# Performance work log

Measured on AMD Instinct MI355X. Metric: run time of the kernel, lower is better.

Reference implementation:

```python
import jax, jax.numpy as jnp
import numpy as np

ALPHA = 0.2  # LeakyReLU negative slope (undefined global `alpha` in source; canonical GAT value)
MASK_VAL = -9e15


def setup_inputs() -> dict:
    key = jax.random.key(0)
    k = jax.random.split(key, 6)
    B, N, D = 8, 2048, 256
    x = jax.random.normal(k[0], (B, N, D), dtype=jnp.float32)
    adj = jax.random.randint(k[1], (B, N, N), 0, 2, dtype=jnp.int32)
    W = jax.random.normal(k[2], (D, D), dtype=jnp.float32) * (1.414 / np.sqrt(D))
    a = jax.random.normal(k[3], (2 * D, 1), dtype=jnp.float32) * 0.1
    han_w = jax.random.normal(k[4], (D, D), dtype=jnp.float32) / np.sqrt(D)
    han_b = jax.random.normal(k[5], (D,), dtype=jnp.float32) * 0.01
    return {"x": x, "adj": adj, "W": W, "a": a, "han_w": han_w, "han_b": han_b}


def reference(x, adj, W, a, han_w, han_b):
    B, N, D = x.shape
    h = jnp.matmul(x, W)                              # [B,N,D]
    a1 = jnp.matmul(x, a[:D])                         # [B,N,1]
    a2 = jnp.matmul(x, a[D:])                         # [B,N,1]
    # e[b,i,j] = leakyrelu(a1[b,i] + a2[b,j])
    e = jax.nn.leaky_relu(a1 + jnp.swapaxes(a2, 1, 2), negative_slope=ALPHA)  # [B,N,N]
    att = jnp.where(adj > 0, e, MASK_VAL)
    # NOTE: source softmaxes over dim=1 (source-node axis), faithfully reproduced
    att = jax.nn.softmax(att, axis=1)
    h_prime = jnp.matmul(att, h)                      # [B,N,D]
    hid = jax.nn.elu(h_prime)                         # concat=True branch
    return jnp.matmul(hid, han_w) + han_b
```

## Files before the change

### kernel.cpp

```cpp
#include <hip/hip_runtime.h>
#include <hip/hip_bf16.h>
#include <stdint.h>

#define B_ 8
#define N_ 2048
#define D_ 256
#define BN (B_*N_)
#define NSEG 64
#define SROWS (N_/NSEG)

typedef __bf16 bf16;
typedef bf16 bf16x8 __attribute__((ext_vector_type(8)));
typedef bf16 bf16x4 __attribute__((ext_vector_type(4)));
typedef float f32x4 __attribute__((ext_vector_type(4)));

__device__ __forceinline__ void gload16(const void* g, void* l) {
  __builtin_amdgcn_global_load_lds(
      (const __attribute__((address_space(1))) unsigned int*)g,
      (__attribute__((address_space(3))) unsigned int*)l,
      16, 0, 0);
}

__global__ __launch_bounds__(256) void k_transpose_w(
    const float* __restrict__ w, const float* __restrict__ hw,
    bf16* __restrict__ wt, bf16* __restrict__ hwt) {
  int t = blockIdx.x * 256 + threadIdx.x;
  int d = t >> 8, k = t & 255;
  wt[t]  = (bf16)w[k * D_ + d];
  hwt[t] = (bf16)hw[k * D_ + d];
}

__global__ __launch_bounds__(256) void k_gemm_h(
    const float* __restrict__ x, const bf16* __restrict__ wt,
    const float* __restrict__ avec, bf16* __restrict__ hT,
    float* __restrict__ a1, float* __restrict__ e1, float* __restrict__ f1,
    float* __restrict__ a2, float* __restrict__ e2, float* __restrict__ f2) {
  int blk = blockIdx.x;
  int b = blk >> 5;
  int j0 = (blk & 31) * 64;
  int w = threadIdx.x >> 6, l = threadIdx.x & 63;
  int jr = j0 + w * 16 + (l & 15);
  const float* xrow = x + ((size_t)(b * N_ + jr)) * D_;
  int koff = 8 * (l >> 4);
  f32x4 acc[16];
  #pragma unroll
  for (int i = 0; i < 16; ++i) acc[i] = f32x4{0.f, 0.f, 0.f, 0.f};
  float s1 = 0.f, s2 = 0.f;
  for (int kb = 0; kb < D_; kb += 32) {
    float4 xa = *(const float4*)(xrow + kb + koff);
    float4 xb = *(const float4*)(xrow + kb + koff + 4);
    float4 ua = *(const float4*)(avec + kb + koff);
    float4 ub = *(const float4*)(avec + kb + koff + 4);
    float4 va = *(const float4*)(avec + D_ + kb + koff);
    float4 vb = *(const float4*)(avec + D_ + kb + koff + 4);
    s1 = fmaf(xa.x, ua.x, fmaf(xa.y, ua.y, fmaf(xa.z, ua.z, fmaf(xa.w, ua.w, s1))));
    s1 = fmaf(xb.x, ub.x, fmaf(xb.y, ub.y, fmaf(xb.z, ub.z, fmaf(xb.w, ub.w, s1))));
    s2 = fmaf(xa.x, va.x, fmaf(xa.y, va.y, fmaf(xa.z, va.z, fmaf(xa.w, va.w, s2))));
    s2 = fmaf(xb.x, vb.x, fmaf(xb.y, vb.y, fmaf(xb.z, vb.z, fmaf(xb.w, vb.w, s2))));
    bf16x8 af = { (bf16)xa.x, (bf16)xa.y, (bf16)xa.z, (bf16)xa.w,
                  (bf16)xb.x, (bf16)xb.y, (bf16)xb.z, (bf16)xb.w };
    #pragma unroll
    for (int dt = 0; dt < 16; ++dt) {
      bf16x8 bfr = *(const bf16x8*)(wt + (dt * 16 + (l & 15)) * D_ + kb + koff);
      acc[dt] = __builtin_amdgcn_mfma_f32_16x16x32_bf16(af, bfr, acc[dt], 0, 0, 0);
    }
  }
  s1 += __shfl_xor(s1, 16); s1 += __shfl_xor(s1, 32);
  s2 += __shfl_xor(s2, 16); s2 += __shfl_xor(s2, 32);
  if (l < 16) {
    int row = b * N_ + j0 + w * 16 + l;
    a1[row] = s1; e1[row] = __expf(s1); f1[row] = __expf(0.2f * s1);
    a2[row] = s2; e2[row] = __expf(s2); f2[row] = __expf(0.2f * s2);
  }
  int jw = j0 + w * 16 + (l >> 4) * 4;
  #pragma unroll
  for (int dt = 0; dt < 16; ++dt) {
    int d = dt * 16 + (l & 15);
    bf16x4 o = { (bf16)acc[dt][0], (bf16)acc[dt][1], (bf16)acc[dt][2], (bf16)acc[dt][3] };
    *(bf16x4*)(hT + ((size_t)(b * D_ + d)) * N_ + jw) = o;
  }
}

__global__ __launch_bounds__(256) void k_colstats(
    const int* __restrict__ adj,
    const float* __restrict__ a1, const float* __restrict__ e1, const float* __restrict__ f1,
    const float* __restrict__ a2,
    float* __restrict__ partA, float* __restrict__ partB,
    unsigned char* __restrict__ maskB) {
  int blk = blockIdx.x;
  int b  = blk >> 6;
  int is = blk & (NSEG - 1);
  int t = threadIdx.x;
  int ibase = is * SROWS;
  __shared__ float a1s[SROWS], e1s[SROWS], f1s[SROWS];
  if (t < SROWS) {
    int gi = b * N_ + ibase + t;
    a1s[t] = a1[gi]; e1s[t] = e1[gi]; f1s[t] = f1[gi];
  }
  __syncthreads();
  int j0 = t * 8;
  float4 a2lo = *(const float4*)(a2 + b * N_ + j0);
  float4 a2hi = *(const float4*)(a2 + b * N_ + j0 + 4);
  float a2v[8] = {a2lo.x, a2lo.y, a2lo.z, a2lo.w, a2hi.x, a2hi.y, a2hi.z, a2hi.w};
  float SA[8], SB[8];
  #pragma unroll
  for (int e = 0; e < 8; ++e) { SA[e] = 0.f; SB[e] = 0.f; }
  const int* arow = adj + ((size_t)(b * N_ + ibase)) * N_ + j0;
  unsigned char* mrow = maskB + (size_t)(b * N_ + ibase) * (N_ / 8) + t;
  #pragma unroll 4
  for (int ii = 0; ii < SROWS; ++ii) {
    int4 v0 = *(const int4*)(arow + (size_t)ii * N_);
    int4 v1 = *(const int4*)(arow + (size_t)ii * N_ + 4);
    float a1i = a1s[ii], e1i = e1s[ii], f1i = f1s[ii];
    int vals[8] = {v0.x, v0.y, v0.z, v0.w, v1.x, v1.y, v1.z, v1.w};
    unsigned int mb = 0;
    #pragma unroll
    for (int e = 0; e < 8; ++e) {
      bool pred = vals[e] != 0;
      mb |= pred ? (1u << e) : 0u;
      float tt = a1i + a2v[e];
      bool gt = tt > 0.f;
      SA[e] += (pred && gt)  ? e1i : 0.f;
      SB[e] += (pred && !gt) ? f1i : 0.f;
    }
    mrow[(size_t)ii * (N_ / 8)] = (unsigned char)mb;
  }
  float* pA = partA + ((size_t)(b * NSEG + is)) * N_ + j0;
  float* pB = partB + ((size_t)(b * NSEG + is)) * N_ + j0;
  *(float4*)(pA)     = float4{SA[0], SA[1], SA[2], SA[3]};
  *(float4*)(pA + 4) = float4{SA[4], SA[5], SA[6], SA[7]};
  *(float4*)(pB)     = float4{SB[0], SB[1], SB[2], SB[3]};
  *(float4*)(pB + 4) = float4{SB[4], SB[5], SB[6], SB[7]};
}

__global__ __launch_bounds__(256) void k_colfin(
    const float* __restrict__ partA, const float* __restrict__ partB,
    const float* __restrict__ e2, const float* __restrict__ f2,
    float* __restrict__ e2rs, float* __restrict__ f2rs) {
  int g = blockIdx.x * 256 + threadIdx.x;
  int b = g >> 11, j = g & (N_ - 1);
  float SA = 0.f, SB = 0.f;
  #pragma unroll 8
  for (int is = 0; is < NSEG; ++is) {
    SA += partA[((size_t)(b * NSEG + is)) * N_ + j];
    SB += partB[((size_t)(b * NSEG + is)) * N_ + j];
  }
  float s = e2[g] * SA + f2[g] * SB;
  float rs = s > 0.f ? 1.f / s : 0.f;
  e2rs[g] = e2[g] * rs;
  f2rs[g] = f2[g] * rs;
}

__global__ __launch_bounds__(512, 2) void k_attmm(
    const bf16* __restrict__ hT, const unsigned char* __restrict__ maskB,
    const float* __restrict__ a1v, const float* __restrict__ e1v, const float* __restrict__ f1v,
    const float* __restrict__ a2v, const float* __restrict__ e2rs, const float* __restrict__ f2rs,
    const bf16* __restrict__ hwt, const float* __restrict__ hb,
    float* __restrict__ out) {
  __shared__ __attribute__((aligned(128))) char smem[120 * 1024];
  char* s_b = smem;
  char* s_a = smem + 65536;
  float* s_src = (float*)(smem + 81920);
  unsigned char* s_mask = (unsigned char*)(smem + 106496);
  char* s_hid = smem;

  int blk = blockIdx.x;
  int b  = blk & 7;
  int i0 = (blk >> 3) * 64;
  int t = threadIdx.x, w = t >> 6, l = t & 63;
  int l15 = l & 15, lg = l >> 4;
  int iw = w & 1, dw = w >> 1;

  #pragma unroll
  for (int s = 0; s < 3; ++s) {
    int idx = t + s * 512;
    int arr = idx >> 9, pos = (idx & 511) * 4;
    const float* src = (arr == 0) ? (a2v + b * N_) : (arr == 1) ? (e2rs + b * N_) : (f2rs + b * N_);
    *(float4*)(s_src + arr * N_ + pos) = *(const float4*)(src + pos);
  }
  {
    int row = t >> 3, seg = t & 7;
    const unsigned long long* g = (const unsigned long long*)
        (maskB + ((size_t)(b * N_ + i0 + row)) * (N_ / 8) + seg * 32);
    int sw = (row & 31) << 3;
    #pragma unroll
    for (int k2 = 0; k2 < 4; ++k2) {
      int cb = seg * 32 + k2 * 8;
      *(unsigned long long*)(s_mask + row * 256 + (cb ^ sw)) = g[k2];
    }
  }

  int ib = t >> 3, jq = t & 7;
  int gi = b * N_ + i0 + ib;
  float a1i = a1v[gi], e1i = e1v[gi], f1i = f1v[gi];
  int mswz = (ib & 31) << 3;
  const unsigned char* mline = s_mask + ib * 256;
  const bf16* hTb = hT + (size_t)b * D_ * N_;

  f32x4 acc[2][4];
  #pragma unroll
  for (int is = 0; is < 2; ++is)
    #pragma unroll
    for (int ds = 0; ds < 4; ++ds) acc[is][ds] = f32x4{0.f, 0.f, 0.f, 0.f};

  __syncthreads();

  #define STAGE_B(KB, NB) do {                                              \
    char* dstb = s_b + (NB) * 32768;                                        \
    _Pragma("unroll")                                                       \
    for (int r = 0; r < 4; ++r) {                                           \
      int c = r * 512 + t;                                                  \
      int dd = c >> 3, sub = c & 7;                                         \
      int ssub = sub ^ (dd & 7);                                            \
      gload16(hTb + (size_t)dd * N_ + (KB) + ssub * 8, dstb + c * 16);      \
    }                                                                       \
  } while (0)

  #define BUILD_A(KB, NB) do {                                              \
    int jb = (KB) + jq * 8;                                                 \
    float4 p0 = *(const float4*)(s_src + jb);                               \
    float4 p1 = *(const float4*)(s_src + jb + 4);                           \
    float4 q0 = *(const float4*)(s_src + N_ + jb);                          \
    float4 q1 = *(const float4*)(s_src + N_ + jb + 4);                      \
    float4 r0 = *(const float4*)(s_src + 2 * N_ + jb);                      \
    float4 r1 = *(const float4*)(s_src + 2 * N_ + jb + 4);                  \
    unsigned int m = mline[((((KB) >> 3) + jq)) ^ mswz];                    \
    float a2x[8] = {p0.x,p0.y,p0.z,p0.w,p1.x,p1.y,p1.z,p1.w};               \
    float evx[8] = {q0.x,q0.y,q0.z,q0.w,q1.x,q1.y,q1.z,q1.w};               \
    float fvx[8] = {r0.x,r0.y,r0.z,r0.w,r1.x,r1.y,r1.z,r1.w};               \
    bf16x8 av;                                                              \
    _Pragma("unroll")                                                       \
    for (int e = 0; e < 8; ++e) {                                           \
      float tt = a1i + a2x[e];                                              \
      bool sel = tt > 0.f;                                                  \
      float vv = (sel ? e1i : f1i) * (sel ? evx[e] : fvx[e]);               \
      vv = ((m >> e) & 1u) ? vv : 0.f;                                      \
      av[e] = (bf16)vv;                                                     \
    }                                                                       \
    *(bf16x8*)(s_a + (NB) * 8192 + ib * 128 + ((jq ^ (ib & 7)) * 16)) = av; \
  } while (0)

  STAGE_B(0, 0);
  BUILD_A(0, 0);
  __syncthreads();

  int cur = 0;
  for (int ks = 0; ks < 32; ++ks) {
    if (ks < 31) {
      int kbn = (ks + 1) * 64;
      STAGE_B(kbn, cur ^ 1);
      BUILD_A(kbn, cur ^ 1);
    }
    const char* sa = s_a + cur * 8192;
    const char* sb = s_b + cur * 32768;
    #pragma unroll
    for (int kh = 0; kh < 2; ++kh) {
      int kq = kh * 4 + lg;
      bf16x8 afr[2], bfr[4];
      #pragma unroll
      for (int is = 0; is < 2; ++is) {
        int ra = iw * 32 + is * 16 + l15;
        afr[is] = *(const bf16x8*)(sa + ra * 128 + ((kq ^ (ra & 7)) * 16));
      }
      #pragma unroll
      for (int ds = 0; ds < 4; ++ds) {
        int rb = dw * 64 + ds * 16 + l15;
        bfr[ds] = *(const bf16x8*)(sb + rb * 128 + ((kq ^ (rb & 7)) * 16));
      }
      #pragma unroll
      for (int is = 0; is < 2; ++is)
        #pragma unroll
        for (int ds = 0; ds < 4; ++ds)
          acc[is][ds] = __builtin_amdgcn_mfma_f32_16x16x32_bf16(
              afr[is], bfr[ds], acc[is][ds], 0, 0, 0);
    }
    __syncthreads();
    cur ^= 1;
  }

  #pragma unroll
  for (int is = 0; is < 2; ++is) {
    #pragma unroll
    for (int ds = 0; ds < 4; ++ds) {
      int d = dw * 64 + ds * 16 + l15;
      int c = d >> 3, dby = (d & 7) * 2;
      #pragma unroll
      for (int r = 0; r < 4; ++r) {
        int il = iw * 32 + is * 16 + lg * 4 + r;
        float vv = acc[is][ds][r];
        float hv = vv > 0.f ? vv : __expf(vv) - 1.f;
        *(bf16*)(s_hid + il * 512 + ((c ^ (il & 31)) * 16) + dby) = (bf16)hv;
      }
    }
  }
  __syncthreads();

  f32x4 acc2[2][4];
  #pragma unroll
  for (int is = 0; is < 2; ++is)
    #pragma unroll
    for (int ds = 0; ds < 4; ++ds) acc2[is][ds] = f32x4{0.f, 0.f, 0.f, 0.f};
  #pragma unroll
  for (int kh = 0; kh < 8; ++kh) {
    int kc = kh * 4 + lg;
    bf16x8 afr2[2];
    #pragma unroll
    for (int is = 0; is < 2; ++is) {
      int ra = iw * 32 + is * 16 + l15;
      afr2[is] = *(const bf16x8*)(s_hid + ra * 512 + ((kc ^ (ra & 31)) * 16));
    }
    #pragma unroll
    for (int ds = 0; ds < 4; ++ds) {
      int d2 = dw * 64 + ds * 16 + l15;
      bf16x8 bfr2 = *(const bf16x8*)(hwt + (size_t)d2 * D_ + kh * 32 + lg * 8);
      #pragma unroll
      for (int is = 0; is < 2; ++is)
        acc2[is][ds] = __builtin_amdgcn_mfma_f32_16x16x32_bf16(
            afr2[is], bfr2, acc2[is][ds], 0, 0, 0);
    }
  }
  #pragma unroll
  for (int is = 0; is < 2; ++is) {
    #pragma unroll
    for (int ds = 0; ds < 4; ++ds) {
      int d = dw * 64 + ds * 16 + l15;
      float bias = hb[d];
      #pragma unroll
      for (int r = 0; r < 4; ++r) {
        int i = i0 + iw * 32 + is * 16 + lg * 4 + r;
        out[((size_t)(b * N_ + i)) * D_ + d] = acc2[is][ds][r] + bias;
      }
    }
  }
}

extern "C" void kernel_launch(void* const* d_in, const int* in_sizes, int n_in,
                              void* d_out, int out_size, void* d_ws, size_t ws_size,
                              hipStream_t stream) {
  (void)in_sizes; (void)n_in; (void)out_size; (void)ws_size;
  const float* x   = (const float*)d_in[0];
  const int*   adj = (const int*)d_in[1];
  const float* W   = (const float*)d_in[2];
  const float* a   = (const float*)d_in[3];
  const float* hw  = (const float*)d_in[4];
  const float* hb  = (const float*)d_in[5];
  float* out = (float*)d_out;

  char* ws = (char*)d_ws;
  size_t off = 0;
  auto alloc = [&](size_t bytes) -> char* {
    char* p = ws + off;
    off += (bytes + 255) & ~(size_t)255;
    return p;
  };
  float* a1   = (float*)alloc(BN * 4);
  float* e1   = (float*)alloc(BN * 4);
  float* f1   = (float*)alloc(BN * 4);
  float* a2   = (float*)alloc(BN * 4);
  float* e2   = (float*)alloc(BN * 4);
  float* f2   = (float*)alloc(BN * 4);
  float* e2rs = (float*)alloc(BN * 4);
  float* f2rs = (float*)alloc(BN * 4);
  float* partA = (float*)alloc((size_t)B_ * NSEG * N_ * 4);
  float* partB = (float*)alloc((size_t)B_ * NSEG * N_ * 4);
  unsigned char* maskB = (unsigned char*)alloc((size_t)BN * (N_ / 8));
  bf16* hT  = (bf16*)alloc((size_t)B_ * D_ * N_ * 2);
  bf16* wt  = (bf16*)alloc((size_t)D_ * D_ * 2);
  bf16* hwt = (bf16*)alloc((size_t)D_ * D_ * 2);

  k_transpose_w<<<256, 256, 0, stream>>>(W, hw, wt, hwt);
  k_gemm_h<<<256, 256, 0, stream>>>(x, wt, a, hT, a1, e1, f1, a2, e2, f2);
  k_colstats<<<B_ * NSEG, 256, 0, stream>>>(adj, a1, e1, f1, a2, partA, partB, maskB);
  k_colfin<<<BN / 256, 256, 0, stream>>>(partA, partB, e2, f2, e2rs, f2rs);
  k_attmm<<<256, 512, 0, stream>>>(hT, maskB, a1, e1, f1, a2, e2rs, f2rs,
                                   hwt, hb, out);
}
```

Before: 111.3 us.

## Split attention matmul K across warp halves with LDS reduction

Changes the warp tiling of the main attention×h MFMA loop. Each warp now covers all 64 rows and a 64-column d slice but only half of each 64-wide k step, instead of half the rows and both k halves. This raises the number of A and B fragments reused per LDS read and packs 16 MFMAs per step into one block. The cost is double the accumulator registers (64 floats) and an extra cross-warp reduction through LDS with an added barrier before the ELU and output matmul.

```diff
diff --git a/kernel.cpp b/kernel.cpp
--- a/kernel.cpp
+++ b/kernel.cpp
@@ -163,13 +163,14 @@
   float* s_src = (float*)(smem + 81920);
   unsigned char* s_mask = (unsigned char*)(smem + 106496);
   char* s_hid = smem;
+  char* s_mrg = smem + 32768;
 
   int blk = blockIdx.x;
   int b  = blk & 7;
   int i0 = (blk >> 3) * 64;
   int t = threadIdx.x, w = t >> 6, l = t & 63;
   int l15 = l & 15, lg = l >> 4;
-  int iw = w & 1, dw = w >> 1;
+  int dwm = w & 3, kh = w >> 2;
 
   #pragma unroll
   for (int s = 0; s < 3; ++s) {
@@ -197,9 +198,9 @@
   const unsigned char* mline = s_mask + ib * 256;
   const bf16* hTb = hT + (size_t)b * D_ * N_;
 
-  f32x4 acc[2][4];
-  #pragma unroll
-  for (int is = 0; is < 2; ++is)
+  f32x4 acc[4][4];
+  #pragma unroll
+  for (int is = 0; is < 4; ++is)
     #pragma unroll
     for (int ds = 0; ds < 4; ++ds) acc[is][ds] = f32x4{0.f, 0.f, 0.f, 0.f};
 
@@ -244,6 +245,7 @@
   BUILD_A(0, 0);
   __syncthreads();
 
+  int kq = kh * 4 + lg;
   int cur = 0;
   for (int ks = 0; ks < 32; ++ks) {
     if (ks < 31) {
@@ -253,66 +255,75 @@
     }
     const char* sa = s_a + cur * 8192;
     const char* sb = s_b + cur * 32768;
-    #pragma unroll
-    for (int kh = 0; kh < 2; ++kh) {
-      int kq = kh * 4 + lg;
-      bf16x8 afr[2], bfr[4];
-      #pragma unroll
-      for (int is = 0; is < 2; ++is) {
-        int ra = iw * 32 + is * 16 + l15;
-        afr[is] = *(const bf16x8*)(sa + ra * 128 + ((kq ^ (ra & 7)) * 16));
-      }
-      #pragma unroll
-      for (int ds = 0; ds < 4; ++ds) {
-        int rb = dw * 64 + ds * 16 + l15;
-        bfr[ds] = *(const bf16x8*)(sb + rb * 128 + ((kq ^ (rb & 7)) * 16));
-      }
-      #pragma unroll
-      for (int is = 0; is < 2; ++is)
-        #pragma unroll
-        for (int ds = 0; ds < 4; ++ds)
-          acc[is][ds] = __builtin_amdgcn_mfma_f32_16x16x32_bf16(
-              afr[is], bfr[ds], acc[is][ds], 0, 0, 0);
-    }
+    bf16x8 afr[4], bfr[4];
+    #pragma unroll
+    for (int is = 0; is < 4; ++is) {
+      int ra = is * 16 + l15;
+      afr[is] = *(const bf16x8*)(sa + ra * 128 + ((kq ^ (ra & 7)) * 16));
+    }
+    #pragma unroll
+    for (int ds = 0; ds < 4; ++ds) {
+      int rb = dwm * 64 + ds * 16 + l15;
+      bfr[ds] = *(const bf16x8*)(sb + rb * 128 + ((kq ^ (rb & 7)) * 16));
+    }
+    #pragma unroll
+    for (int is = 0; is < 4; ++is)
+      #pragma unroll
+      for (int ds = 0; ds < 4; ++ds)
+        acc[is][ds] = __builtin_amdgcn_mfma_f32_16x16x32_bf16(
+            afr[is], bfr[ds], acc[is][ds], 0, 0, 0);
     __syncthreads();
     cur ^= 1;
   }
 
-  #pragma unroll
-  for (int is = 0; is < 2; ++is) {
+  if (kh == 1) {
+    #pragma unroll
+    for (int is = 0; is < 4; ++is)
+      #pragma unroll
+      for (int ds = 0; ds < 4; ++ds)
+        *(f32x4*)(s_mrg + (size_t)dwm * 16384 + ((is * 4 + ds) * 64 + l) * 16) = acc[is][ds];
+  }
+  __syncthreads();
+  if (kh == 0) {
+    #pragma unroll
+    for (int is = 0; is < 4; ++is) {
+      #pragma unroll
+      for (int ds = 0; ds < 4; ++ds) {
+        f32x4 o = *(const f32x4*)(s_mrg + (size_t)dwm * 16384 + ((is * 4 + ds) * 64 + l) * 16);
+        f32x4 sm = acc[is][ds] + o;
+        int d = dwm * 64 + ds * 16 + l15;
+        int c = d >> 3, dby = (d & 7) * 2;
+        #pragma unroll
+        for (int r = 0; r < 4; ++r) {
+          int il = is * 16 + lg * 4 + r;
+          float vv = sm[r];
+          float hv = vv > 0.f ? vv : __expf(vv) - 1.f;
+          *(bf16*)(s_hid + il * 512 + ((c ^ (il & 31)) * 16) + dby) = (bf16)hv;
+        }
+      }
+    }
+  }
+  __syncthreads();
+
+  int iw2 = w & 1, dw2 = w >> 1;
+  f32x4 acc2[2][4];
+  #pragma unroll
+  for (int is = 0; is < 2; ++is)
+    #pragma unroll
+    for (int ds = 0; ds < 4; ++ds) acc2[is][ds] = f32x4{0.f, 0.f, 0.f, 0.f};
+  #pragma unroll
+  for (int kh2 = 0; kh2 < 8; ++kh2) {
+    int kc = kh2 * 4 + lg;
+    bf16x8 afr2[2];
+    #pragma unroll
+    for (int is = 0; is < 2; ++is) {
+      int ra = iw2 * 32 + is * 16 + l15;
+      afr2[is] = *(const bf16x8*)(s_hid + ra * 512 + ((kc ^ (ra & 31)) * 16));
+    }
     #pragma unroll
     for (int ds = 0; ds < 4; ++ds) {
-      int d = dw * 64 + ds * 16 + l15;
-      int c = d >> 3, dby = (d & 7) * 2;
-      #pragma unroll
-      for (int r = 0; r < 4; ++r) {
-        int il = iw * 32 + is * 16 + lg * 4 + r;
-        float vv = acc[is][ds][r];
-        float hv = vv > 0.f ? vv : __expf(vv) - 1.f;
-        *(bf16*)(s_hid + il * 512 + ((c ^ (il & 31)) * 16) + dby) = (bf16)hv;
-      }
-    }
-  }
-  __syncthreads();
-
-  f32x4 acc2[2][4];
-  #pragma unroll
-  for (int is = 0; is < 2; ++is)
-    #pragma unroll
-    for (int ds = 0; ds < 4; ++ds) acc2[is][ds] = f32x4{0.f, 0.f, 0.f, 0.f};
-  #pragma unroll
-  for (int kh = 0; kh < 8; ++kh) {
-    int kc = kh * 4 + lg;
-    bf16x8 afr2[2];
-    #pragma unroll
-    for (int is = 0; is < 2; ++is) {
-      int ra = iw * 32 + is * 16 + l15;
-      afr2[is] = *(const bf16x8*)(s_hid + ra * 512 + ((kc ^ (ra & 31)) * 16));
-    }
-    #pragma unroll
-    for (int ds = 0; ds < 4; ++ds) {
-      int d2 = dw * 64 + ds * 16 + l15;
-      bf16x8 bfr2 = *(const bf16x8*)(hwt + (size_t)d2 * D_ + kh * 32 + lg * 8);
+      int d2 = dw2 * 64 + ds * 16 + l15;
+      bf16x8 bfr2 = *(const bf16x8*)(hwt + (size_t)d2 * D_ + kh2 * 32 + lg * 8);
       #pragma unroll
       for (int is = 0; is < 2; ++is)
         acc2[is][ds] = __builtin_amdgcn_mfma_f32_16x16x32_bf16(
@@ -323,11 +334,11 @@
   for (int is = 0; is < 2; ++is) {
     #pragma unroll
     for (int ds = 0; ds < 4; ++ds) {
-      int d = dw * 64 + ds * 16 + l15;
+      int d = dw2 * 64 + ds * 16 + l15;
       float bias = hb[d];
       #pragma unroll
       for (int r = 0; r < 4; ++r) {
-        int i = i0 + iw * 32 + is * 16 + lg * 4 + r;
+        int i = i0 + iw2 * 32 + is * 16 + lg * 4 + r;
         out[((size_t)(b * N_ + i)) * D_ + d] = acc2[is][ds][r] + bias;
       }
     }
```

Result: no change. 111.9 us (+0.6%).

## Materialize bf16 attention matrix in separate kernel and split colstats rows across thread groups

Applied to the files above, without the earlier changes.

Moves construction of the masked, normalized attention weights out of the GEMM kernel into a new kernel that writes a full bf16 attention matrix to global memory. The GEMM then stages A tiles with async global-to-LDS loads, which cuts its LDS use and raises the occupancy hint. Separately, colstats now uses 512 threads, with two groups each covering 16 rows and an LDS reduction before the partial sums are written. The new approach adds a 64 MB write plus reread of the attention matrix in exchange for a simpler, less ALU-heavy GEMM inner loop.

```diff
diff --git a/kernel.cpp b/kernel.cpp
--- a/kernel.cpp
+++ b/kernel.cpp
@@ -7,7 +7,7 @@
 #define D_ 256
 #define BN (B_*N_)
 #define NSEG 64
-#define SROWS (N_/NSEG)
+#define SROWS 32
 
 typedef __bf16 bf16;
 typedef bf16 bf16x8 __attribute__((ext_vector_type(8)));
@@ -81,7 +81,7 @@
   }
 }
 
-__global__ __launch_bounds__(256) void k_colstats(
+__global__ __launch_bounds__(512) void k_colstats(
     const int* __restrict__ adj,
     const float* __restrict__ a1, const float* __restrict__ e1, const float* __restrict__ f1,
     const float* __restrict__ a2,
@@ -91,14 +91,16 @@
   int b  = blk >> 6;
   int is = blk & (NSEG - 1);
   int t = threadIdx.x;
-  int ibase = is * SROWS;
+  int grp = t >> 8, tt = t & 255;
+  int ibase = is * SROWS + grp * 16;
   __shared__ float a1s[SROWS], e1s[SROWS], f1s[SROWS];
+  __shared__ float redA[256 * 8], redB[256 * 8];
   if (t < SROWS) {
-    int gi = b * N_ + ibase + t;
+    int gi = b * N_ + is * SROWS + t;
     a1s[t] = a1[gi]; e1s[t] = e1[gi]; f1s[t] = f1[gi];
   }
   __syncthreads();
-  int j0 = t * 8;
+  int j0 = tt * 8;
   float4 a2lo = *(const float4*)(a2 + b * N_ + j0);
   float4 a2hi = *(const float4*)(a2 + b * N_ + j0 + 4);
   float a2v[8] = {a2lo.x, a2lo.y, a2lo.z, a2lo.w, a2hi.x, a2hi.y, a2hi.z, a2hi.w};
@@ -106,31 +108,41 @@
   #pragma unroll
   for (int e = 0; e < 8; ++e) { SA[e] = 0.f; SB[e] = 0.f; }
   const int* arow = adj + ((size_t)(b * N_ + ibase)) * N_ + j0;
-  unsigned char* mrow = maskB + (size_t)(b * N_ + ibase) * (N_ / 8) + t;
+  unsigned char* mrow = maskB + (size_t)(b * N_ + ibase) * (N_ / 8) + tt;
   #pragma unroll 4
-  for (int ii = 0; ii < SROWS; ++ii) {
+  for (int ii = 0; ii < 16; ++ii) {
     int4 v0 = *(const int4*)(arow + (size_t)ii * N_);
     int4 v1 = *(const int4*)(arow + (size_t)ii * N_ + 4);
-    float a1i = a1s[ii], e1i = e1s[ii], f1i = f1s[ii];
+    int sr = grp * 16 + ii;
+    float a1i = a1s[sr], e1i = e1s[sr], f1i = f1s[sr];
     int vals[8] = {v0.x, v0.y, v0.z, v0.w, v1.x, v1.y, v1.z, v1.w};
     unsigned int mb = 0;
     #pragma unroll
     for (int e = 0; e < 8; ++e) {
       bool pred = vals[e] != 0;
       mb |= pred ? (1u << e) : 0u;
-      float tt = a1i + a2v[e];
-      bool gt = tt > 0.f;
+      float ttv = a1i + a2v[e];
+      bool gt = ttv > 0.f;
       SA[e] += (pred && gt)  ? e1i : 0.f;
       SB[e] += (pred && !gt) ? f1i : 0.f;
     }
     mrow[(size_t)ii * (N_ / 8)] = (unsigned char)mb;
   }
-  float* pA = partA + ((size_t)(b * NSEG + is)) * N_ + j0;
-  float* pB = partB + ((size_t)(b * NSEG + is)) * N_ + j0;
-  *(float4*)(pA)     = float4{SA[0], SA[1], SA[2], SA[3]};
-  *(float4*)(pA + 4) = float4{SA[4], SA[5], SA[6], SA[7]};
-  *(float4*)(pB)     = float4{SB[0], SB[1], SB[2], SB[3]};
-  *(float4*)(pB + 4) = float4{SB[4], SB[5], SB[6], SB[7]};
+  if (grp == 1) {
+    #pragma unroll
+    for (int e = 0; e < 8; ++e) { redA[tt * 8 + e] = SA[e]; redB[tt * 8 + e] = SB[e]; }
+  }
+  __syncthreads();
+  if (grp == 0) {
+    #pragma unroll
+    for (int e = 0; e < 8; ++e) { SA[e] += redA[tt * 8 + e]; SB[e] += redB[tt * 8 + e]; }
+    float* pA = partA + ((size_t)(b * NSEG + is)) * N_ + j0;
+    float* pB = partB + ((size_t)(b * NSEG + is)) * N_ + j0;
+    *(float4*)(pA)     = float4{SA[0], SA[1], SA[2], SA[3]};
+    *(float4*)(pA + 4) = float4{SA[4], SA[5], SA[6], SA[7]};
+    *(float4*)(pB)     = float4{SB[0], SB[1], SB[2], SB[3]};
+    *(float4*)(pB + 4) = float4{SB[4], SB[5], SB[6], SB[7]};
+  }
 }
 
 __global__ __launch_bounds__(256) void k_colfin(
@@ -151,17 +163,48 @@
   f2rs[g] = f2[g] * rs;
 }
 
-__global__ __launch_bounds__(512, 2) void k_attmm(
-    const bf16* __restrict__ hT, const unsigned char* __restrict__ maskB,
-    const float* __restrict__ a1v, const float* __restrict__ e1v, const float* __restrict__ f1v,
-    const float* __restrict__ a2v, const float* __restrict__ e2rs, const float* __restrict__ f2rs,
+__global__ __launch_bounds__(512) void k_attbuild(
+    const unsigned char* __restrict__ maskB,
+    const float* __restrict__ a1, const float* __restrict__ e1, const float* __restrict__ f1,
+    const float* __restrict__ a2, const float* __restrict__ e2rs, const float* __restrict__ f2rs,
+    bf16* __restrict__ att) {
+  int g = blockIdx.x * 512 + threadIdx.x;
+  int row = g >> 8;
+  int j0 = (g & 255) * 8;
+  int b = row >> 11;
+  float a1i = a1[row], e1i = e1[row], f1i = f1[row];
+  const float* a2b = a2 + b * N_;
+  const float* eb  = e2rs + b * N_;
+  const float* fb  = f2rs + b * N_;
+  unsigned int mb = maskB[(size_t)row * (N_ / 8) + (j0 >> 3)];
+  float4 p0 = *(const float4*)(a2b + j0);
+  float4 p1 = *(const float4*)(a2b + j0 + 4);
+  float4 q0 = *(const float4*)(eb + j0);
+  float4 q1 = *(const float4*)(eb + j0 + 4);
+  float4 r0 = *(const float4*)(fb + j0);
+  float4 r1 = *(const float4*)(fb + j0 + 4);
+  float a2x[8] = {p0.x,p0.y,p0.z,p0.w,p1.x,p1.y,p1.z,p1.w};
+  float evx[8] = {q0.x,q0.y,q0.z,q0.w,q1.x,q1.y,q1.z,q1.w};
+  float fvx[8] = {r0.x,r0.y,r0.z,r0.w,r1.x,r1.y,r1.z,r1.w};
+  bf16x8 av;
+  #pragma unroll
+  for (int e = 0; e < 8; ++e) {
+    float tt = a1i + a2x[e];
+    bool sel = tt > 0.f;
+    float vv = (sel ? e1i : f1i) * (sel ? evx[e] : fvx[e]);
+    vv = ((mb >> e) & 1u) ? vv : 0.f;
+    av[e] = (bf16)vv;
+  }
+  *(bf16x8*)(att + (size_t)row * N_ + j0) = av;
+}
+
+__global__ __launch_bounds__(512, 4) void k_attmm(
+    const bf16* __restrict__ att, const bf16* __restrict__ hT,
     const bf16* __restrict__ hwt, const float* __restrict__ hb,
     float* __restrict__ out) {
-  __shared__ __attribute__((aligned(128))) char smem[120 * 1024];
+  __shared__ __attribute__((aligned(128))) char smem[80 * 1024];
   char* s_b = smem;
   char* s_a = smem + 65536;
-  float* s_src = (float*)(smem + 81920);
-  unsigned char* s_mask = (unsigned char*)(smem + 106496);
   char* s_hid = smem;
 
   int blk = blockIdx.x;
@@ -171,39 +214,14 @@
   int l15 = l & 15, lg = l >> 4;
   int iw = w & 1, dw = w >> 1;
 
-  #pragma unroll
-  for (int s = 0; s < 3; ++s) {
-    int idx = t + s * 512;
-    int arr = idx >> 9, pos = (idx & 511) * 4;
-    const float* src = (arr == 0) ? (a2v + b * N_) : (arr == 1) ? (e2rs + b * N_) : (f2rs + b * N_);
-    *(float4*)(s_src + arr * N_ + pos) = *(const float4*)(src + pos);
-  }
-  {
-    int row = t >> 3, seg = t & 7;
-    const unsigned long long* g = (const unsigned long long*)
-        (maskB + ((size_t)(b * N_ + i0 + row)) * (N_ / 8) + seg * 32);
-    int sw = (row & 31) << 3;
-    #pragma unroll
-    for (int k2 = 0; k2 < 4; ++k2) {
-      int cb = seg * 32 + k2 * 8;
-      *(unsigned long long*)(s_mask + row * 256 + (cb ^ sw)) = g[k2];
-    }
-  }
-
-  int ib = t >> 3, jq = t & 7;
-  int gi = b * N_ + i0 + ib;
-  float a1i = a1v[gi], e1i = e1v[gi], f1i = f1v[gi];
-  int mswz = (ib & 31) << 3;
-  const unsigned char* mline = s_mask + ib * 256;
   const bf16* hTb = hT + (size_t)b * D_ * N_;
+  const bf16* attB = att + (size_t)b * N_ * N_ + (size_t)i0 * N_;
 
   f32x4 acc[2][4];
   #pragma unroll
   for (int is = 0; is < 2; ++is)
     #pragma unroll
     for (int ds = 0; ds < 4; ++ds) acc[is][ds] = f32x4{0.f, 0.f, 0.f, 0.f};
-
-  __syncthreads();
 
   #define STAGE_B(KB, NB) do {                                              \
     char* dstb = s_b + (NB) * 32768;                                        \
@@ -216,40 +234,24 @@
     }                                                                       \
   } while (0)
 
-  #define BUILD_A(KB, NB) do {                                              \
-    int jb = (KB) + jq * 8;                                                 \
-    float4 p0 = *(const float4*)(s_src + jb);                               \
-    float4 p1 = *(const float4*)(s_src + jb + 4);                           \
-    float4 q0 = *(const float4*)(s_src + N_ + jb);                          \
-    float4 q1 = *(const float4*)(s_src + N_ + jb + 4);                      \
-    float4 r0 = *(const float4*)(s_src + 2 * N_ + jb);                      \
-    float4 r1 = *(const float4*)(s_src + 2 * N_ + jb + 4);                  \
-    unsigned int m = mline[((((KB) >> 3) + jq)) ^ mswz];                    \
-    float a2x[8] = {p0.x,p0.y,p0.z,p0.w,p1.x,p1.y,p1.z,p1.w};               \
-    float evx[8] = {q0.x,q0.y,q0.z,q0.w,q1.x,q1.y,q1.z,q1.w};               \
-    float fvx[8] = {r0.x,r0.y,r0.z,r0.w,r1.x,r1.y,r1.z,r1.w};               \
-    bf16x8 av;                                                              \
-    _Pragma("unroll")                                                       \
-    for (int e = 0; e < 8; ++e) {                                           \
-      float tt = a1i + a2x[e];                                              \
-      bool sel = tt > 0.f;                                                  \
-      float vv = (sel ? e1i : f1i) * (sel ? evx[e] : fvx[e]);               \
-      vv = ((m >> e) & 1u) ? vv : 0.f;                                      \
-      av[e] = (bf16)vv;                                                     \
-    }                                                                       \
-    *(bf16x8*)(s_a + (NB) * 8192 + ib * 128 + ((jq ^ (ib & 7)) * 16)) = av; \
+  #define STAGE_A(KB, NB) do {                                              \
+    char* dsta = s_a + (NB) * 8192;                                         \
+    int c = t;                                                              \
+    int ia = c >> 3, sub = c & 7;                                           \
+    int ssub = sub ^ (ia & 7);                                              \
+    gload16(attB + (size_t)ia * N_ + (KB) + ssub * 8, dsta + c * 16);       \
   } while (0)
 
+  STAGE_A(0, 0);
   STAGE_B(0, 0);
-  BUILD_A(0, 0);
   __syncthreads();
 
   int cur = 0;
   for (int ks = 0; ks < 32; ++ks) {
     if (ks < 31) {
       int kbn = (ks + 1) * 64;
+      STAGE_A(kbn, cur ^ 1);
       STAGE_B(kbn, cur ^ 1);
-      BUILD_A(kbn, cur ^ 1);
     }
     const char* sa = s_a + cur * 8192;
     const char* sb = s_b + cur * 32768;
@@ -365,13 +367,14 @@
   float* partB = (float*)alloc((size_t)B_ * NSEG * N_ * 4);
   unsigned char* maskB = (unsigned char*)alloc((size_t)BN * (N_ / 8));
   bf16* hT  = (bf16*)alloc((size_t)B_ * D_ * N_ * 2);
+  bf16* att = (bf16*)alloc((size_t)B_ * N_ * N_ * 2);
   bf16* wt  = (bf16*)alloc((size_t)D_ * D_ * 2);
   bf16* hwt = (bf16*)alloc((size_t)D_ * D_ * 2);
 
   k_transpose_w<<<256, 256, 0, stream>>>(W, hw, wt, hwt);
   k_gemm_h<<<256, 256, 0, stream>>>(x, wt, a, hT, a1, e1, f1, a2, e2, f2);
-  k_colstats<<<B_ * NSEG, 256, 0, stream>>>(adj, a1, e1, f1, a2, partA, partB, maskB);
+  k_colstats<<<B_ * NSEG, 512, 0, stream>>>(adj, a1, e1, f1, a2, partA, partB, maskB);
   k_colfin<<<BN / 256, 256, 0, stream>>>(partA, partB, e2, f2, e2rs, f2rs);
-  k_attmm<<<256, 512, 0, stream>>>(hT, maskB, a1, e1, f1, a2, e2rs, f2rs,
-                                   hwt, hb, out);
-}
+  k_attbuild<<<BN * 256 / 512, 512, 0, stream>>>(maskB, a1, e1, f1, a2, e2rs, f2rs, att);
+  k_attmm<<<256, 512, 0, stream>>>(att, hT, hwt, hb, out);
+}
```

New measurement: 121.6 us. +9.3%, slower.
